# Kernel optimization log

Measured on AMD Instinct MI355X. Metric: run time of the kernel, lower is better.

## Reference

```python
import jax, jax.numpy as jnp
import numpy as np

V, BLOCK, L, H, E, B, T = 1024, 2048, 4, 8, 512, 4, 2048
D = E // H  # head dim = 64

def setup_inputs() -> dict:
    key = jax.random.key(0)
    ks = jax.random.split(key, 8)
    s = 0.02
    return {
        "idx": jax.random.randint(ks[0], (B, T), 0, V),
        "wte": jax.random.normal(ks[1], (V, E), jnp.float32) * s,
        "wpe": jax.random.normal(ks[2], (BLOCK, E), jnp.float32) * s,
        "ln1_w": jnp.ones((L, E), jnp.float32),
        "ln1_b": jnp.zeros((L, E), jnp.float32),
        "attn_w": jax.random.normal(ks[3], (L, 3 * E, E), jnp.float32) * s,
        "attn_b": jnp.zeros((L, 3 * E), jnp.float32),
        "proj_w": jax.random.normal(ks[4], (L, E, E), jnp.float32) * s,
        "proj_b": jnp.zeros((L, E), jnp.float32),
        "ln2_w": jnp.ones((L, E), jnp.float32),
        "ln2_b": jnp.zeros((L, E), jnp.float32),
        "fc_w": jax.random.normal(ks[5], (L, 4 * E, E), jnp.float32) * s,
        "fc_b": jnp.zeros((L, 4 * E), jnp.float32),
        "fc2_w": jax.random.normal(ks[6], (L, E, 4 * E), jnp.float32) * s,
        "fc2_b": jnp.zeros((L, E), jnp.float32),
        "lnf_w": jnp.ones((E,), jnp.float32),
        "lnf_b": jnp.zeros((E,), jnp.float32),
    }

def layer_norm(x, w, b, eps=1e-5):
    mu = jnp.mean(x, axis=-1, keepdims=True)
    var = jnp.var(x, axis=-1, keepdims=True)
    return (x - mu) * jax.lax.rsqrt(var + eps) * w + b

def reference(idx, wte, wpe, ln1_w, ln1_b, attn_w, attn_b, proj_w, proj_b,
              ln2_w, ln2_b, fc_w, fc_b, fc2_w, fc2_b, lnf_w, lnf_b):
    b, t = idx.shape
    x = wte[idx] + wpe[:t]  # (B,T,E)
    causal = jnp.tril(jnp.ones((t, t), bool))
    scale = 1.0 / np.sqrt(D)

    def block(x, p):
        l1w, l1b, aw, ab, pw, pb, l2w, l2b, fw, fb, f2w, f2b = p
        h = layer_norm(x, l1w, l1b)
        qkv = h @ aw.T + ab  # (B,T,3E)
        q, k, v = jnp.split(qkv, 3, axis=-1)
        q = q.reshape(b, t, H, D)
        k = k.reshape(b, t, H, D)
        v = v.reshape(b, t, H, D)
        att = jnp.einsum('bqhd,bkhd->bhqk', q, k) * scale
        att = jnp.where(causal, att, -jnp.inf)
        att = jax.nn.softmax(att, axis=-1)
        y = jnp.einsum('bhqk,bkhd->bqhd', att, v).reshape(b, t, E)
        x = x + y @ pw.T + pb
        h2 = layer_norm(x, l2w, l2b)
        h2 = jax.nn.gelu(h2 @ fw.T + fb, approximate=False)
        x = x + h2 @ f2w.T + f2b
        return x, None

    params = (ln1_w, ln1_b, attn_w, attn_b, proj_w, proj_b,
              ln2_w, ln2_b, fc_w, fc_b, fc2_w, fc2_b)
    x, _ = jax.lax.scan(block, x, params)
    x = layer_norm(x, lnf_w, lnf_b)
    logits = x @ wte.T  # tied lm_head
    return logits
```

## Files before the change

kernel.cpp:

```cpp
#include <hip/hip_runtime.h>
#include <hip/hip_bf16.h>
#include <math.h>

#define B_ 4
#define T_ 2048
#define E_ 512
#define H_ 8
#define D_ 64
#define L_ 4
#define V_ 1024
#define NROWS (B_*T_)
#define KBLK 64
#define KVPAD 72
#define PPAD 72

typedef __hip_bfloat16 bf16;
typedef __attribute__((ext_vector_type(8))) short bf16x8;
typedef __attribute__((ext_vector_type(4))) float f32x4;

__device__ __forceinline__ short f2bf_s(float f) {
    union { bf16 h; short s; } t; t.h = __float2bfloat16(f); return t.s;
}

__device__ __forceinline__ void gload_lds16(const bf16* g, bf16* l) {
    __builtin_amdgcn_global_load_lds((const __attribute__((address_space(1))) void*)g,
                                     (__attribute__((address_space(3))) void*)l, 16, 0, 0);
}

__device__ __forceinline__ float gelu_fast(float v) {
    float u = v * (0.7978845608028654f * (1.0f + 0.044715f * v * v));
    float t = 1.0f - 2.0f / (__expf(2.0f * u) + 1.0f);
    return 0.5f * v * (1.0f + t);
}

__global__ void f2bf_all(const float* __restrict__ s0, const float* __restrict__ s1,
                         const float* __restrict__ s2, const float* __restrict__ s3,
                         const float* __restrict__ s4, bf16* __restrict__ dst) {
    size_t gi = (size_t)blockIdx.x * 1024 + threadIdx.x * 4;
    const float* src; size_t off;
    if (blockIdx.x < 3072)       { src = s0; off = gi; }
    else if (blockIdx.x < 4096)  { src = s1; off = gi - (size_t)3072 * 1024; }
    else if (blockIdx.x < 8192)  { src = s2; off = gi - (size_t)4096 * 1024; }
    else if (blockIdx.x < 12288) { src = s3; off = gi - (size_t)8192 * 1024; }
    else                         { src = s4; off = gi - (size_t)12288 * 1024; }
    float4 v = *(const float4*)(src + off);
    union { bf16 h[4]; uint2 u; } t;
    t.h[0] = __float2bfloat16(v.x); t.h[1] = __float2bfloat16(v.y);
    t.h[2] = __float2bfloat16(v.z); t.h[3] = __float2bfloat16(v.w);
    *(uint2*)(dst + gi) = t.u;
}

__global__ void embed_kernel(const int* __restrict__ idx, const float* __restrict__ wte,
                             const float* __restrict__ wpe, float* __restrict__ x) {
    int i = (blockIdx.x * blockDim.x + threadIdx.x) * 4;
    int row = i >> 9;
    int e = i & (E_ - 1);
    int t = row & (T_ - 1);
    int id = idx[row];
    float4 a = *(const float4*)(wte + (size_t)id * E_ + e);
    float4 p = *(const float4*)(wpe + (size_t)t * E_ + e);
    a.x += p.x; a.y += p.y; a.z += p.z; a.w += p.w;
    *(float4*)(x + i) = a;
}

__global__ __launch_bounds__(512) void layernorm_kernel(const float* __restrict__ x,
                                 const float* __restrict__ w, const float* __restrict__ b,
                                 bf16* __restrict__ out) {
    int wid = threadIdx.x >> 6, lane = threadIdx.x & 63;
    int row = blockIdx.x * 8 + wid;
    const float* xr = x + (size_t)row * E_ + lane * 8;
    float4 a0 = *(const float4*)xr;
    float4 a1 = *(const float4*)(xr + 4);
    float s = (a0.x + a0.y) + (a0.z + a0.w) + (a1.x + a1.y) + (a1.z + a1.w);
    float q = a0.x*a0.x + a0.y*a0.y + a0.z*a0.z + a0.w*a0.w
            + a1.x*a1.x + a1.y*a1.y + a1.z*a1.z + a1.w*a1.w;
    #pragma unroll
    for (int st = 1; st < 64; st <<= 1) { s += __shfl_xor(s, st); q += __shfl_xor(q, st); }
    float mean = s * (1.0f / E_);
    float var = q * (1.0f / E_) - mean * mean;
    float rstd = rsqrtf(var + 1e-5f);
    float4 w0 = *(const float4*)(w + lane * 8), w1 = *(const float4*)(w + lane * 8 + 4);
    float4 b0 = *(const float4*)(b + lane * 8), b1 = *(const float4*)(b + lane * 8 + 4);
    union { bf16 h[8]; uint4 u; } o;
    o.h[0] = __float2bfloat16((a0.x - mean) * rstd * w0.x + b0.x);
    o.h[1] = __float2bfloat16((a0.y - mean) * rstd * w0.y + b0.y);
    o.h[2] = __float2bfloat16((a0.z - mean) * rstd * w0.z + b0.z);
    o.h[3] = __float2bfloat16((a0.w - mean) * rstd * w0.w + b0.w);
    o.h[4] = __float2bfloat16((a1.x - mean) * rstd * w1.x + b1.x);
    o.h[5] = __float2bfloat16((a1.y - mean) * rstd * w1.y + b1.y);
    o.h[6] = __float2bfloat16((a1.z - mean) * rstd * w1.z + b1.z);
    o.h[7] = __float2bfloat16((a1.w - mean) * rstd * w1.w + b1.w);
    *(uint4*)(out + (size_t)row * E_ + lane * 8) = o.u;
}

template<int ACT, int OMODE, bool BIAS>
__global__ __launch_bounds__(256) void gemm_mfma(const bf16* __restrict__ A, const bf16* __restrict__ W,
        const float* __restrict__ bias, float* __restrict__ Cf, bf16* __restrict__ Cb,
        int M, int N, int K) {
    __shared__ __align__(16) bf16 As[2][128][32];
    __shared__ __align__(16) bf16 Bs[2][128][32];
    int tid = threadIdx.x;
    int lane = tid & 63, wid = tid >> 6;
    int wm = (wid >> 1) * 64, wn = (wid & 1) * 64;
    int m0 = blockIdx.y * 128, n0 = blockIdx.x * 128;

    int srow = wid * 32 + (lane >> 2);
    int scol = (lane & 3) * 8;
    const bf16* ga = A + (size_t)(m0 + srow) * K + scol;
    const bf16* gb = W + (size_t)(n0 + srow) * K + scol;
    int fr = lane & 15, fk = (lane >> 4) * 8;

    f32x4 acc[4][4];
    #pragma unroll
    for (int i = 0; i < 4; ++i)
        #pragma unroll
        for (int j = 0; j < 4; ++j) acc[i][j] = (f32x4){0.f, 0.f, 0.f, 0.f};

    gload_lds16(ga,          &As[0][wid * 32][0]);
    gload_lds16(ga + 16 * K, &As[0][wid * 32 + 16][0]);
    gload_lds16(gb,          &Bs[0][wid * 32][0]);
    gload_lds16(gb + 16 * K, &Bs[0][wid * 32 + 16][0]);
    __syncthreads();

    const int nst = K >> 5;
    for (int t = 0; t < nst; ++t) {
        const int cur = t & 1;
        if (t + 1 < nst) {
            const bf16* ga2 = ga + (t + 1) * 32;
            const bf16* gb2 = gb + (t + 1) * 32;
            gload_lds16(ga2,          &As[cur ^ 1][wid * 32][0]);
            gload_lds16(ga2 + 16 * K, &As[cur ^ 1][wid * 32 + 16][0]);
            gload_lds16(gb2,          &Bs[cur ^ 1][wid * 32][0]);
            gload_lds16(gb2 + 16 * K, &Bs[cur ^ 1][wid * 32 + 16][0]);
        }
        bf16x8 af[4], bff[4];
        #pragma unroll
        for (int i = 0; i < 4; ++i) af[i]  = *(const bf16x8*)&As[cur][wm + i * 16 + fr][fk];
        #pragma unroll
        for (int j = 0; j < 4; ++j) bff[j] = *(const bf16x8*)&Bs[cur][wn + j * 16 + fr][fk];
        #pragma unroll
        for (int i = 0; i < 4; ++i)
            #pragma unroll
            for (int j = 0; j < 4; ++j)
                acc[i][j] = __builtin_amdgcn_mfma_f32_16x16x32_bf16(af[i], bff[j], acc[i][j], 0, 0, 0);
        __syncthreads();
    }

    int orow = m0 + wm + (lane >> 4) * 4;
    int ocol = n0 + wn + (lane & 15);
    #pragma unroll
    for (int i = 0; i < 4; ++i) {
        #pragma unroll
        for (int j = 0; j < 4; ++j) {
            #pragma unroll
            for (int r = 0; r < 4; ++r) {
                int row = orow + i * 16 + r;
                int col = ocol + j * 16;
                float v = acc[i][j][r];
                if (BIAS) v += bias[col];
                if (ACT == 1) v = gelu_fast(v);
                size_t off = (size_t)row * N + col;
                if (OMODE == 0) Cf[off] = v;
                else if (OMODE == 1) Cb[off] = __float2bfloat16(v);
                else Cf[off] += v;
            }
        }
    }
}

template<int OMODE, bool BIAS, bool QKV>
__global__ __launch_bounds__(256) void gemm_mfma64(const bf16* __restrict__ A, const bf16* __restrict__ W,
        const float* __restrict__ bias, float* __restrict__ Cf, bf16* __restrict__ Cb,
        bf16* __restrict__ Vt, int M, int N, int K) {
    __shared__ __align__(16) bf16 As[2][64][32];
    __shared__ __align__(16) bf16 Bs[2][64][32];
    int tid = threadIdx.x;
    int lane = tid & 63, wid = tid >> 6;
    int wm = (wid >> 1) * 32, wn = (wid & 1) * 32;
    int m0 = blockIdx.y * 64, n0 = blockIdx.x * 64;

    int srow = wid * 16 + (lane >> 2);
    int scol = (lane & 3) * 8;
    const bf16* ga = A + (size_t)(m0 + srow) * K + scol;
    const bf16* gb = W + (size_t)(n0 + srow) * K + scol;
    int fr = lane & 15, fk = (lane >> 4) * 8;

    f32x4 acc[2][2];
    #pragma unroll
    for (int i = 0; i < 2; ++i)
        #pragma unroll
        for (int j = 0; j < 2; ++j) acc[i][j] = (f32x4){0.f, 0.f, 0.f, 0.f};

    gload_lds16(ga, &As[0][wid * 16][0]);
    gload_lds16(gb, &Bs[0][wid * 16][0]);
    __syncthreads();

    const int nst = K >> 5;
    for (int t = 0; t < nst; ++t) {
        const int cur = t & 1;
        if (t + 1 < nst) {
            gload_lds16(ga + (t + 1) * 32, &As[cur ^ 1][wid * 16][0]);
            gload_lds16(gb + (t + 1) * 32, &Bs[cur ^ 1][wid * 16][0]);
        }
        bf16x8 af[2], bff[2];
        #pragma unroll
        for (int i = 0; i < 2; ++i) af[i]  = *(const bf16x8*)&As[cur][wm + i * 16 + fr][fk];
        #pragma unroll
        for (int j = 0; j < 2; ++j) bff[j] = *(const bf16x8*)&Bs[cur][wn + j * 16 + fr][fk];
        #pragma unroll
        for (int i = 0; i < 2; ++i)
            #pragma unroll
            for (int j = 0; j < 2; ++j)
                acc[i][j] = __builtin_amdgcn_mfma_f32_16x16x32_bf16(af[i], bff[j], acc[i][j], 0, 0, 0);
        __syncthreads();
    }

    int orow = m0 + wm + (lane >> 4) * 4;
    int ocol = n0 + wn + (lane & 15);

    if (QKV && n0 >= 2 * E_) {
        #pragma unroll
        for (int i = 0; i < 2; ++i) {
            int rowb = orow + i * 16;
            int bb = rowb >> 11;
            int t0 = rowb & (T_ - 1);
            #pragma unroll
            for (int j = 0; j < 2; ++j) {
                int col = ocol + j * 16;
                int dg = col - 2 * E_;
                int hh = dg >> 6, dd = dg & 63;
                float bv = BIAS ? bias[col] : 0.0f;
                union { bf16 h[4]; short4 s4; } pk;
                #pragma unroll
                for (int r = 0; r < 4; ++r)
                    pk.h[r] = __float2bfloat16(acc[i][j][r] + bv);
                *(short4*)&Vt[(((size_t)bb * H_ + hh) * D_ + dd) * T_ + t0] = pk.s4;
            }
        }
        return;
    }

    #pragma unroll
    for (int i = 0; i < 2; ++i) {
        #pragma unroll
        for (int j = 0; j < 2; ++j) {
            #pragma unroll
            for (int r = 0; r < 4; ++r) {
                int row = orow + i * 16 + r;
                int col = ocol + j * 16;
                float v = acc[i][j][r];
                if (BIAS) v += bias[col];
                if (QKV) {
                    if (col < E_) v *= 0.125f;
                    Cb[(size_t)row * (2 * E_) + col] = __float2bfloat16(v);
                } else {
                    size_t off = (size_t)row * N + col;
                    if (OMODE == 0) Cf[off] = v;
                    else if (OMODE == 1) Cb[off] = __float2bfloat16(v);
                    else Cf[off] += v;
                }
            }
        }
    }
}

template<bool DOMASK>
__device__ __forceinline__ void attn_tile(
        const short (&Ks)[KBLK][KVPAD], const short (&VsT)[D_][KVPAD],
        short (*Psw)[PPAD], const bf16x8 (&qf)[2],
        float& m_run, float& l_run, f32x4 (&accO)[4],
        int fr, int fg, int k0, int qrow) {
    f32x4 st[4];
    __builtin_amdgcn_s_setprio(1);
    #pragma unroll
    for (int j = 0; j < 4; ++j) {
        f32x4 a = (f32x4){0.f, 0.f, 0.f, 0.f};
        #pragma unroll
        for (int kk = 0; kk < 2; ++kk) {
            bf16x8 kf = *(const bf16x8*)&Ks[j * 16 + fr][kk * 32 + fg * 8];
            a = __builtin_amdgcn_mfma_f32_16x16x32_bf16(kf, qf[kk], a, 0, 0, 0);
        }
        st[j] = a;
    }
    __builtin_amdgcn_s_setprio(0);
    float mx = -INFINITY;
    #pragma unroll
    for (int j = 0; j < 4; ++j)
        #pragma unroll
        for (int r = 0; r < 4; ++r) {
            if (DOMASK && (k0 + j * 16 + fg * 4 + r > qrow)) st[j][r] = -INFINITY;
            mx = fmaxf(mx, st[j][r]);
        }
    mx = fmaxf(mx, __shfl_xor(mx, 16));
    mx = fmaxf(mx, __shfl_xor(mx, 32));
    if (!__all(mx <= m_run + 8.0f)) {
        float mnew = fmaxf(m_run, mx);
        float corr = __expf(m_run - mnew);
        l_run *= corr;
        #pragma unroll
        for (int r = 0; r < 4; ++r) {
            float cr = __shfl(corr, fg * 4 + r);
            #pragma unroll
            for (int n = 0; n < 4; ++n) accO[n][r] *= cr;
        }
        m_run = mnew;
    }
    float rl = 0.0f;
    #pragma unroll
    for (int j = 0; j < 4; ++j) {
        float p0 = __expf(st[j][0] - m_run), p1 = __expf(st[j][1] - m_run);
        float p2 = __expf(st[j][2] - m_run), p3 = __expf(st[j][3] - m_run);
        rl += (p0 + p1) + (p2 + p3);
        short4 pk;
        pk.x = f2bf_s(p0); pk.y = f2bf_s(p1); pk.z = f2bf_s(p2); pk.w = f2bf_s(p3);
        *(short4*)&Psw[fr][j * 16 + fg * 4] = pk;
    }
    rl += __shfl_xor(rl, 16);
    rl += __shfl_xor(rl, 32);
    l_run += rl;
    __builtin_amdgcn_s_setprio(1);
    bf16x8 pa[2];
    #pragma unroll
    for (int kk = 0; kk < 2; ++kk)
        pa[kk] = *(const bf16x8*)&Psw[fr][kk * 32 + fg * 8];
    #pragma unroll
    for (int n = 0; n < 4; ++n)
        #pragma unroll
        for (int kk = 0; kk < 2; ++kk) {
            bf16x8 vb = *(const bf16x8*)&VsT[n * 16 + fr][kk * 32 + fg * 8];
            accO[n] = __builtin_amdgcn_mfma_f32_16x16x32_bf16(pa[kk], vb, accO[n], 0, 0, 0);
        }
    __builtin_amdgcn_s_setprio(0);
}

__global__ __launch_bounds__(256, 3) void attn_mfma(const bf16* __restrict__ qk,
                                                    const bf16* __restrict__ vt,
                                                    bf16* __restrict__ y) {
    __shared__ __align__(16) short Ks[2][KBLK][KVPAD];
    __shared__ __align__(16) short VsT[2][D_][KVPAD];
    __shared__ __align__(16) short Ps[4][16][PPAD];
    const int qi = (gridDim.x - 1) - blockIdx.x;
    const int h = blockIdx.y, b = blockIdx.z;
    const int q0 = qi * 64;
    const int tid = threadIdx.x;
    const int lane = tid & 63, wid = tid >> 6;
    const int fr = lane & 15, fg = lane >> 4;
    const int qmin = q0 + wid * 16;
    const int qrow = qmin + fr;

    const int sr0 = tid >> 3;
    const int sc = (tid & 7) * 8;
    const bf16* kst = qk + (size_t)(b * T_ + sr0) * (2 * E_) + E_ + h * D_ + sc;
    const bf16* vst = vt + ((size_t)(b * H_ + h) * D_ + sr0) * T_ + sc;

    const bf16* qbase = qk + (size_t)(b * T_ + qrow) * (2 * E_) + h * D_;
    bf16x8 qf[2];
    #pragma unroll
    for (int kk = 0; kk < 2; ++kk)
        qf[kk] = *(const bf16x8*)(qbase + kk * 32 + fg * 8);

    float m_run = -INFINITY, l_run = 0.0f;
    f32x4 accO[4];
    #pragma unroll
    for (int n = 0; n < 4; ++n) accO[n] = (f32x4){0.f, 0.f, 0.f, 0.f};

    const int ntiles = qi + 1;

    {
        uint4 k0r = *(const uint4*)kst;
        uint4 k1r = *(const uint4*)(kst + 32 * (2 * E_));
        uint4 v0r = *(const uint4*)vst;
        uint4 v1r = *(const uint4*)(vst + 32 * T_);
        *(uint4*)&Ks[0][sr0][sc] = k0r;  *(uint4*)&Ks[0][sr0 + 32][sc] = k1r;
        *(uint4*)&VsT[0][sr0][sc] = v0r; *(uint4*)&VsT[0][sr0 + 32][sc] = v1r;
    }
    __syncthreads();

    for (int kt = 0; kt < ntiles; ++kt) {
        const int cur = kt & 1;
        const bool have_next = (kt + 1 < ntiles);
        uint4 nk0, nk1, nv0, nv1;
        if (have_next) {
            const bf16* kn = kst + (size_t)(kt + 1) * KBLK * (2 * E_);
            const bf16* vn = vst + (kt + 1) * KBLK;
            nk0 = *(const uint4*)kn; nk1 = *(const uint4*)(kn + 32 * (2 * E_));
            nv0 = *(const uint4*)vn; nv1 = *(const uint4*)(vn + 32 * T_);
        }

        if (kt + 1 == ntiles)
            attn_tile<true >(Ks[cur], VsT[cur], Ps[wid], qf, m_run, l_run, accO, fr, fg, kt * KBLK, qrow);
        else
            attn_tile<false>(Ks[cur], VsT[cur], Ps[wid], qf, m_run, l_run, accO, fr, fg, kt * KBLK, qrow);

        if (have_next) {
            const int nxt = cur ^ 1;
            *(uint4*)&Ks[nxt][sr0][sc] = nk0;  *(uint4*)&Ks[nxt][sr0 + 32][sc] = nk1;
            *(uint4*)&VsT[nxt][sr0][sc] = nv0; *(uint4*)&VsT[nxt][sr0 + 32][sc] = nv1;
        }
        __syncthreads();
    }

    float linv = 1.0f / l_run;
    #pragma unroll
    for (int r = 0; r < 4; ++r) {
        float lr = __shfl(linv, fg * 4 + r);
        int gq = qmin + fg * 4 + r;
        #pragma unroll
        for (int n = 0; n < 4; ++n)
            y[(size_t)(b * T_ + gq) * E_ + h * D_ + n * 16 + fr] =
                __float2bfloat16(accO[n][r] * lr);
    }
}

extern "C" void kernel_launch(void* const* d_in, const int* in_sizes, int n_in,
                              void* d_out, int out_size, void* d_ws, size_t ws_size,
                              hipStream_t stream) {
    const int*   idx    = (const int*)d_in[0];
    const float* wte    = (const float*)d_in[1];
    const float* wpe    = (const float*)d_in[2];
    const float* ln1_w  = (const float*)d_in[3];
    const float* ln1_b  = (const float*)d_in[4];
    const float* attn_w = (const float*)d_in[5];
    const float* attn_b = (const float*)d_in[6];
    const float* proj_w = (const float*)d_in[7];
    const float* proj_b = (const float*)d_in[8];
    const float* ln2_w  = (const float*)d_in[9];
    const float* ln2_b  = (const float*)d_in[10];
    const float* fc_w   = (const float*)d_in[11];
    const float* fc_b   = (const float*)d_in[12];
    const float* fc2_w  = (const float*)d_in[13];
    const float* fc2_b  = (const float*)d_in[14];
    const float* lnf_w  = (const float*)d_in[15];
    const float* lnf_b  = (const float*)d_in[16];
    float* out = (float*)d_out;

    float* x   = (float*)d_ws;
    bf16* hbf  = (bf16*)(x + (size_t)NROWS * E_);
    bf16* big  = hbf + (size_t)NROWS * E_;
    bf16* qkb  = big;
    bf16* vtb  = big + (size_t)NROWS * 2 * E_;
    bf16* wb   = big + (size_t)NROWS * 4 * E_;
    bf16* attn_wb = wb;
    bf16* proj_wb = attn_wb + (size_t)L_ * 3 * E_ * E_;
    bf16* fc_wb   = proj_wb + (size_t)L_ * E_ * E_;
    bf16* fc2_wb  = fc_wb   + (size_t)L_ * 4 * E_ * E_;
    bf16* wte_b   = fc2_wb  + (size_t)L_ * E_ * 4 * E_;

    f2bf_all<<<12800, 256, 0, stream>>>(attn_w, proj_w, fc_w, fc2_w, wte, wb);
    embed_kernel<<<NROWS * E_ / 1024, 256, 0, stream>>>(idx, wte, wpe, x);

    for (int l = 0; l < L_; ++l) {
        layernorm_kernel<<<NROWS / 8, 512, 0, stream>>>(x, ln1_w + l * E_, ln1_b + l * E_, hbf);
        gemm_mfma64<1, true, true><<<dim3(3 * E_ / 64, NROWS / 64), 256, 0, stream>>>(
            hbf, attn_wb + (size_t)l * 3 * E_ * E_, attn_b + l * 3 * E_, nullptr, qkb, vtb,
            NROWS, 3 * E_, E_);
        attn_mfma<<<dim3(T_ / 64, H_, B_), 256, 0, stream>>>(qkb, vtb, hbf);
        gemm_mfma64<2, true, false><<<dim3(E_ / 64, NROWS / 64), 256, 0, stream>>>(
            hbf, proj_wb + (size_t)l * E_ * E_, proj_b + l * E_, x, nullptr, nullptr,
            NROWS, E_, E_);
        layernorm_kernel<<<NROWS / 8, 512, 0, stream>>>(x, ln2_w + l * E_, ln2_b + l * E_, hbf);
        gemm_mfma<1, 1, true><<<dim3(4 * E_ / 128, NROWS / 128), 256, 0, stream>>>(
            hbf, fc_wb + (size_t)l * 4 * E_ * E_, fc_b + l * 4 * E_, nullptr, big,
            NROWS, 4 * E_, E_);
        gemm_mfma64<2, true, false><<<dim3(E_ / 64, NROWS / 64), 256, 0, stream>>>(
            big, fc2_wb + (size_t)l * E_ * 4 * E_, fc2_b + l * E_, x, nullptr, nullptr,
            NROWS, E_, 4 * E_);
    }
    layernorm_kernel<<<NROWS / 8, 512, 0, stream>>>(x, lnf_w, lnf_b, hbf);
    gemm_mfma64<0, false, false><<<dim3(V_ / 64, NROWS / 64), 256, 0, stream>>>(
        hbf, wte_b, nullptr, out, nullptr, nullptr, NROWS, V_, E_);
}
```

Baseline: 955.8 us.

## Deepen GEMM K-step to 64 and single-buffer attention LDS for occupancy

The 64x64 GEMM now stages two 32-wide K slices per pipeline stage, which halves the number of loop iterations and barriers while doubling LDS per block. The attention kernel drops its double-buffered K/V shared tiles in favour of a single buffer with an extra barrier per tile, and raises the launch-bounds occupancy hint from 3 to 4 blocks. Prefetching into registers is kept, so global latency is still overlapped. The extra barrier serializes the LDS store against compute, and the tighter register budget from the higher occupancy hint could cause spills.

```diff
diff --git a/kernel.cpp b/kernel.cpp
--- a/kernel.cpp
+++ b/kernel.cpp
@@ -172,8 +172,8 @@
 __global__ __launch_bounds__(256) void gemm_mfma64(const bf16* __restrict__ A, const bf16* __restrict__ W,
         const float* __restrict__ bias, float* __restrict__ Cf, bf16* __restrict__ Cb,
         bf16* __restrict__ Vt, int M, int N, int K) {
-    __shared__ __align__(16) bf16 As[2][64][32];
-    __shared__ __align__(16) bf16 Bs[2][64][32];
+    __shared__ __align__(16) bf16 As[2][2][64][32];
+    __shared__ __align__(16) bf16 Bs[2][2][64][32];
     int tid = threadIdx.x;
     int lane = tid & 63, wid = tid >> 6;
     int wm = (wid >> 1) * 32, wn = (wid & 1) * 32;
@@ -191,27 +191,36 @@
         #pragma unroll
         for (int j = 0; j < 2; ++j) acc[i][j] = (f32x4){0.f, 0.f, 0.f, 0.f};
 
-    gload_lds16(ga, &As[0][wid * 16][0]);
-    gload_lds16(gb, &Bs[0][wid * 16][0]);
+    gload_lds16(ga,      &As[0][0][wid * 16][0]);
+    gload_lds16(ga + 32, &As[0][1][wid * 16][0]);
+    gload_lds16(gb,      &Bs[0][0][wid * 16][0]);
+    gload_lds16(gb + 32, &Bs[0][1][wid * 16][0]);
     __syncthreads();
 
-    const int nst = K >> 5;
+    const int nst = K >> 6;
     for (int t = 0; t < nst; ++t) {
         const int cur = t & 1;
         if (t + 1 < nst) {
-            gload_lds16(ga + (t + 1) * 32, &As[cur ^ 1][wid * 16][0]);
-            gload_lds16(gb + (t + 1) * 32, &Bs[cur ^ 1][wid * 16][0]);
-        }
-        bf16x8 af[2], bff[2];
-        #pragma unroll
-        for (int i = 0; i < 2; ++i) af[i]  = *(const bf16x8*)&As[cur][wm + i * 16 + fr][fk];
-        #pragma unroll
-        for (int j = 0; j < 2; ++j) bff[j] = *(const bf16x8*)&Bs[cur][wn + j * 16 + fr][fk];
-        #pragma unroll
-        for (int i = 0; i < 2; ++i)
-            #pragma unroll
-            for (int j = 0; j < 2; ++j)
-                acc[i][j] = __builtin_amdgcn_mfma_f32_16x16x32_bf16(af[i], bff[j], acc[i][j], 0, 0, 0);
+            const bf16* ga2 = ga + (t + 1) * 64;
+            const bf16* gb2 = gb + (t + 1) * 64;
+            gload_lds16(ga2,      &As[cur ^ 1][0][wid * 16][0]);
+            gload_lds16(ga2 + 32, &As[cur ^ 1][1][wid * 16][0]);
+            gload_lds16(gb2,      &Bs[cur ^ 1][0][wid * 16][0]);
+            gload_lds16(gb2 + 32, &Bs[cur ^ 1][1][wid * 16][0]);
+        }
+        #pragma unroll
+        for (int s = 0; s < 2; ++s) {
+            bf16x8 af[2], bff[2];
+            #pragma unroll
+            for (int i = 0; i < 2; ++i) af[i]  = *(const bf16x8*)&As[cur][s][wm + i * 16 + fr][fk];
+            #pragma unroll
+            for (int j = 0; j < 2; ++j) bff[j] = *(const bf16x8*)&Bs[cur][s][wn + j * 16 + fr][fk];
+            #pragma unroll
+            for (int i = 0; i < 2; ++i)
+                #pragma unroll
+                for (int j = 0; j < 2; ++j)
+                    acc[i][j] = __builtin_amdgcn_mfma_f32_16x16x32_bf16(af[i], bff[j], acc[i][j], 0, 0, 0);
+        }
         __syncthreads();
     }
 
@@ -333,11 +342,11 @@
     __builtin_amdgcn_s_setprio(0);
 }
 
-__global__ __launch_bounds__(256, 3) void attn_mfma(const bf16* __restrict__ qk,
+__global__ __launch_bounds__(256, 4) void attn_mfma(const bf16* __restrict__ qk,
                                                     const bf16* __restrict__ vt,
                                                     bf16* __restrict__ y) {
-    __shared__ __align__(16) short Ks[2][KBLK][KVPAD];
-    __shared__ __align__(16) short VsT[2][D_][KVPAD];
+    __shared__ __align__(16) short Ks[KBLK][KVPAD];
+    __shared__ __align__(16) short VsT[D_][KVPAD];
     __shared__ __align__(16) short Ps[4][16][PPAD];
     const int qi = (gridDim.x - 1) - blockIdx.x;
     const int h = blockIdx.y, b = blockIdx.z;
@@ -371,13 +380,12 @@
         uint4 k1r = *(const uint4*)(kst + 32 * (2 * E_));
         uint4 v0r = *(const uint4*)vst;
         uint4 v1r = *(const uint4*)(vst + 32 * T_);
-        *(uint4*)&Ks[0][sr0][sc] = k0r;  *(uint4*)&Ks[0][sr0 + 32][sc] = k1r;
-        *(uint4*)&VsT[0][sr0][sc] = v0r; *(uint4*)&VsT[0][sr0 + 32][sc] = v1r;
+        *(uint4*)&Ks[sr0][sc] = k0r;  *(uint4*)&Ks[sr0 + 32][sc] = k1r;
+        *(uint4*)&VsT[sr0][sc] = v0r; *(uint4*)&VsT[sr0 + 32][sc] = v1r;
     }
     __syncthreads();
 
     for (int kt = 0; kt < ntiles; ++kt) {
-        const int cur = kt & 1;
         const bool have_next = (kt + 1 < ntiles);
         uint4 nk0, nk1, nv0, nv1;
         if (have_next) {
@@ -388,16 +396,16 @@
         }
 
         if (kt + 1 == ntiles)
-            attn_tile<true >(Ks[cur], VsT[cur], Ps[wid], qf, m_run, l_run, accO, fr, fg, kt * KBLK, qrow);
+            attn_tile<true >(Ks, VsT, Ps[wid], qf, m_run, l_run, accO, fr, fg, kt * KBLK, qrow);
         else
-            attn_tile<false>(Ks[cur], VsT[cur], Ps[wid], qf, m_run, l_run, accO, fr, fg, kt * KBLK, qrow);
-
+            attn_tile<false>(Ks, VsT, Ps[wid], qf, m_run, l_run, accO, fr, fg, kt * KBLK, qrow);
+
+        __syncthreads();
         if (have_next) {
-            const int nxt = cur ^ 1;
-            *(uint4*)&Ks[nxt][sr0][sc] = nk0;  *(uint4*)&Ks[nxt][sr0 + 32][sc] = nk1;
-            *(uint4*)&VsT[nxt][sr0][sc] = nv0; *(uint4*)&VsT[nxt][sr0 + 32][sc] = nv1;
-        }
-        __syncthreads();
+            *(uint4*)&Ks[sr0][sc] = nk0;  *(uint4*)&Ks[sr0 + 32][sc] = nk1;
+            *(uint4*)&VsT[sr0][sc] = nv0; *(uint4*)&VsT[sr0 + 32][sc] = nv1;
+            __syncthreads();
+        }
     }
 
     float linv = 1.0f / l_run;
```

After: 849.0 us. -11.2%, faster.
